# Kernel optimization log

Hardware: AMD Instinct MI355X
Metric: run time of the kernel (lower is better)

## Reference

```python
import jax, jax.numpy as jnp
import numpy as np

BETA = 0.1
TRUNC = 1.0
MIN_VALID_RATIO = 0.3


def _wls_affine(x, y, w):
    # Weighted least squares fit of y ~ s*x + t over the last axis.
    sw = w.sum(-1)
    swx = (w * x).sum(-1)
    swy = (w * y).sum(-1)
    swxx = (w * x * x).sum(-1)
    swxy = (w * x * y).sum(-1)
    det = sw * swxx - swx * swx
    det = jnp.where(jnp.abs(det) < 1e-12, 1e-12, det)
    s = (sw * swxy - swx * swy) / det
    t = (swxx * swy - swx * swxy) / det
    return s, t


def _align_depth_affine(x, y, w, trunc):
    # Truncated robust affine alignment: initial WLS fit, then refit with
    # weights of points whose weighted residual exceeds `trunc` zeroed out
    # (falling back to the original weights if everything is truncated).
    s0, t0 = _wls_affine(x, y, w)
    e = w * jnp.abs(s0[..., None] * x + t0[..., None] - y)
    w2 = w * (e < trunc).astype(w.dtype)
    w2 = jnp.where(w2.sum(-1, keepdims=True) > 1e-8, w2, w)
    return _wls_affine(x, y, w2)


def _smooth(err, beta):
    if beta == 0:
        return err
    return jnp.where(err < beta, 0.5 * err * err / beta, err - 0.5 * beta)


def setup_inputs() -> dict:
    key = jax.random.key(0)
    k1, k2, k3 = jax.random.split(key, 3)
    B = 8
    P = 4096  # num_patches
    K = 256   # patch_pixel_count
    N = P * K
    pred_depth = jax.random.uniform(k1, (B, N), jnp.float32, 0.05, 5.0)
    gt_depth = jax.random.uniform(k2, (B, N), jnp.float32, 0.05, 5.0)
    mask = jax.random.bernoulli(k3, 0.8, (B, N))
    global_scale = jnp.ones((B,), jnp.float32)
    return {
        "pred_depth": pred_depth,
        "gt_depth": gt_depth,
        "mask": mask,
        "global_scale": global_scale,
        "num_patches": P,
        "patch_pixel_count": K,
    }


def reference(pred_depth, gt_depth, mask, global_scale, num_patches, patch_pixel_count):
    B = pred_depth.shape[0]
    P, K = num_patches, patch_pixel_count
    x = pred_depth.reshape(B, P, K)
    y = gt_depth.reshape(B, P, K)
    m = mask.reshape(B, P, K).astype(x.dtype)

    valid_ratio = m.mean(-1)                      # (B, P)
    msum = m.sum(-1)
    mean_depth = jnp.where(msum > 0, (y * m).sum(-1) / jnp.maximum(msum, 1.0), 1.0)

    w = m / jnp.maximum(y, 1e-5)                  # alignment weights (B, P, K)
    s, t = _align_depth_affine(x, y, w, TRUNC)    # (B, P) scale / shift per patch

    ratio = s / jnp.maximum(global_scale[:, None], 1e-12)
    gs_ok = jnp.where(global_scale[:, None] > 0, (ratio >= 0.1) & (ratio <= 10.0), True)
    valid = (valid_ratio >= MIN_VALID_RATIO) & (s > 0) & gs_ok  # (B, P)

    aligned = s[..., None] * x + t[..., None]
    pw = m / jnp.maximum(y, 0.1 * mean_depth[..., None])
    patch_loss = _smooth(jnp.abs(aligned - y) * pw, BETA).mean(-1)  # (B, P)

    vf = valid.astype(x.dtype)
    cnt = vf.sum()
    loss = jnp.where(cnt > 0, (patch_loss * vf).sum() / jnp.maximum(cnt, 1.0), 0.0)
    return loss
```

## Files before the change

### kernel.cpp

```cpp
#include <hip/hip_runtime.h>


#define WPB 4
#define PPW 4
#define MAXBLK 1024

__device__ __forceinline__ float wredu(float v) {
#define DPP_ADD(ctrl)                                                        \
  v += __int_as_float(__builtin_amdgcn_update_dpp(                           \
      0, __float_as_int(v), (ctrl), 0xf, 0xf, true))
  DPP_ADD(0x111);
  DPP_ADD(0x112);
  DPP_ADD(0x114);
  DPP_ADD(0x118);
  DPP_ADD(0x142);
  DPP_ADD(0x143);
#undef DPP_ADD
  return __int_as_float(__builtin_amdgcn_readlane(__float_as_int(v), 63));
}

__device__ __forceinline__ float rowredu(float v) {
#define DPP_ADD(ctrl)                                                        \
  v += __int_as_float(__builtin_amdgcn_update_dpp(                           \
      0, __float_as_int(v), (ctrl), 0xf, 0xf, true))
  DPP_ADD(0x121);
  DPP_ADD(0x122);
  DPP_ADD(0x124);
  DPP_ADD(0x128);
#undef DPP_ADD
  return v;
}

__device__ __forceinline__ float frcp(float x) {
  return __builtin_amdgcn_rcpf(x);
}

__global__ __launch_bounds__(256) void moge_patch_kernel(
    const float* __restrict__ xg,
    const float* __restrict__ yg,
    const int*   __restrict__ mg,
    const float* __restrict__ gsg,
    const int*   __restrict__ pP,
    const int*   __restrict__ pK,
    int B,
    float* __restrict__ ws) {
  const int P = pP[0];
  const int K = pK[0];
  const int lane = threadIdx.x & 63;
  const int wib  = threadIdx.x >> 6;
  const int total_patches = B * P;
  const float invK = 1.0f / (float)K;

  float wloss = 0.f, wcnt = 0.f;

  if (K == 256) {
    const int row = lane >> 4;
    const int col = lane & 15;
    const int poff = col * 16;
    const int wave_stride = gridDim.x * WPB * PPW;

    int pbase = (blockIdx.x * WPB + wib) * PPW;
    if (pbase < total_patches) {
      float4 xa[4], ya[4]; int4 ma[4];
      {
        const int patch0 = pbase + row;
        const long base =
            ((patch0 < total_patches) ? (long)patch0 * 256L : 0L) + poff;
        #pragma unroll
        for (int j = 0; j < 4; ++j) {
          xa[j] = *(const float4*)(xg + base + 4 * j);
          ya[j] = *(const float4*)(yg + base + 4 * j);
          ma[j] = *(const int4*)(mg + base + 4 * j);
        }
      }

      for (;;) {
        const int nbase_p = pbase + wave_stride;
        const bool has_next = nbase_p < total_patches;
        float4 nxa[4], nya[4]; int4 nma[4];
        {
          const int np = nbase_p + row;
          const long nb =
              ((has_next && np < total_patches) ? (long)np * 256L : 0L) + poff;
          #pragma unroll
          for (int j = 0; j < 4; ++j) {
            nxa[j] = *(const float4*)(xg + nb + 4 * j);
            nya[j] = *(const float4*)(yg + nb + 4 * j);
            nma[j] = *(const int4*)(mg + nb + 4 * j);
          }
        }

        const int patch = pbase + row;
        const bool row_ok = patch < total_patches;
        const float* xr = (const float*)xa;
        const float* yr = (const float*)ya;
        const int*   mi = (const int*)ma;
        float wv[16];

        float sw = 0.f, swx = 0.f, swy = 0.f, swxx = 0.f, swxy = 0.f;
        float msum = 0.f, symsum = 0.f;
        #pragma unroll
        for (int i = 0; i < 16; ++i) {
          const float m = mi[i] ? 1.f : 0.f;
          const float xx = xr[i], yy = yr[i];
          const float w = m * frcp(fmaxf(yy, 1e-5f));
          wv[i] = w;
          const float wx = w * xx;
          sw += w; swx += wx; swy = fmaf(w, yy, swy);
          swxx = fmaf(wx, xx, swxx); swxy = fmaf(wx, yy, swxy);
          msum += m; symsum = fmaf(m, yy, symsum);
        }
        sw = rowredu(sw); swx = rowredu(swx); swy = rowredu(swy);
        swxx = rowredu(swxx); swxy = rowredu(swxy);

        float det = sw * swxx - swx * swx;
        if (fabsf(det) < 1e-12f) det = 1e-12f;
        float rdet = frcp(det);
        const float s0 = (sw * swxy - swx * swy) * rdet;
        const float t0 = (swxx * swy - swx * swxy) * rdet;

        float sw2 = 0.f, swx2 = 0.f, swy2 = 0.f, swxx2 = 0.f, swxy2 = 0.f;
        #pragma unroll
        for (int i = 0; i < 16; ++i) {
          const float xx = xr[i], yy = yr[i], w = wv[i];
          const float e = w * fabsf(fmaf(s0, xx, t0) - yy);
          const float w2 = (e < 1.0f) ? w : 0.f;
          const float w2x = w2 * xx;
          sw2 += w2; swx2 += w2x; swy2 = fmaf(w2, yy, swy2);
          swxx2 = fmaf(w2x, xx, swxx2); swxy2 = fmaf(w2x, yy, swxy2);
        }
        sw2 = rowredu(sw2); swx2 = rowredu(swx2); swy2 = rowredu(swy2);
        swxx2 = rowredu(swxx2); swxy2 = rowredu(swxy2);
        msum = rowredu(msum); symsum = rowredu(symsum);

        if (sw2 > 1e-8f) {
          sw = sw2; swx = swx2; swy = swy2; swxx = swxx2; swxy = swxy2;
        }
        det = sw * swxx - swx * swx;
        if (fabsf(det) < 1e-12f) det = 1e-12f;
        rdet = frcp(det);
        const float s = (sw * swxy - swx * swy) * rdet;
        const float t = (swxx * swy - swx * swxy) * rdet;

        const float mean_depth =
            (msum > 0.f) ? (symsum * frcp(fmaxf(msum, 1.f))) : 1.f;
        const float yfloor = 0.1f * mean_depth;

        float lsum = 0.f;
        #pragma unroll
        for (int i = 0; i < 16; ++i) {
          const float m = (wv[i] > 0.f) ? 1.f : 0.f;
          const float pw = m * frcp(fmaxf(yr[i], yfloor));
          const float err = fabsf(fmaf(s, xr[i], t) - yr[i]) * pw;
          lsum += (err < 0.1f) ? (5.0f * err * err) : (err - 0.05f);
        }
        const float patch_loss = rowredu(lsum) * invK;

        const int pidx = row_ok ? patch : (total_patches - 1);
        const float gs = gsg[(unsigned)pidx / (unsigned)P];
        const float ratio = s * frcp(fmaxf(gs, 1e-12f));
        const bool gs_ok = (gs > 0.f) ? (ratio >= 0.1f && ratio <= 10.0f) : true;
        const bool valid = (msum * invK >= 0.3f) && (s > 0.f) && gs_ok;

        if (col == 0 && row_ok && valid) { wloss += patch_loss; wcnt += 1.f; }

        if (!has_next) break;
        pbase = nbase_p;
        #pragma unroll
        for (int j = 0; j < 4; ++j) { xa[j] = nxa[j]; ya[j] = nya[j]; ma[j] = nma[j]; }
      }
    }
  } else {
    const int wave_stride = gridDim.x * WPB;
    for (int patch = blockIdx.x * WPB + wib; patch < total_patches;
         patch += wave_stride) {
      const long base = (long)patch * (long)K;
      const float* xp = xg + base;
      const float* yp = yg + base;
      const int*   mp = mg + base;

      float sw = 0.f, swx = 0.f, swy = 0.f, swxx = 0.f, swxy = 0.f;
      float msum = 0.f, symsum = 0.f;
      for (int j = lane; j < K; j += 64) {
        const float m = mp[j] ? 1.f : 0.f;
        const float xx = xp[j], yy = yp[j];
        const float w = m * frcp(fmaxf(yy, 1e-5f));
        const float wx = w * xx;
        sw += w; swx += wx; swy = fmaf(w, yy, swy);
        swxx = fmaf(wx, xx, swxx); swxy = fmaf(wx, yy, swxy);
        msum += m; symsum = fmaf(m, yy, symsum);
      }
      sw = wredu(sw); swx = wredu(swx); swy = wredu(swy);
      swxx = wredu(swxx); swxy = wredu(swxy);
      msum = wredu(msum); symsum = wredu(symsum);

      float det = sw * swxx - swx * swx;
      if (fabsf(det) < 1e-12f) det = 1e-12f;
      float rdet = frcp(det);
      const float s0 = (sw * swxy - swx * swy) * rdet;
      const float t0 = (swxx * swy - swx * swxy) * rdet;

      float sw2 = 0.f, swx2 = 0.f, swy2 = 0.f, swxx2 = 0.f, swxy2 = 0.f;
      for (int j = lane; j < K; j += 64) {
        const float m = mp[j] ? 1.f : 0.f;
        const float xx = xp[j], yy = yp[j];
        const float w = m * frcp(fmaxf(yy, 1e-5f));
        const float e = w * fabsf(fmaf(s0, xx, t0) - yy);
        const float w2 = (e < 1.0f) ? w : 0.f;
        const float w2x = w2 * xx;
        sw2 += w2; swx2 += w2x; swy2 = fmaf(w2, yy, swy2);
        swxx2 = fmaf(w2x, xx, swxx2); swxy2 = fmaf(w2x, yy, swxy2);
      }
      sw2 = wredu(sw2); swx2 = wredu(swx2); swy2 = wredu(swy2);
      swxx2 = wredu(swxx2); swxy2 = wredu(swxy2);

      if (sw2 > 1e-8f) {
        sw = sw2; swx = swx2; swy = swy2; swxx = swxx2; swxy = swxy2;
      }
      det = sw * swxx - swx * swx;
      if (fabsf(det) < 1e-12f) det = 1e-12f;
      rdet = frcp(det);
      const float s = (sw * swxy - swx * swy) * rdet;
      const float t = (swxx * swy - swx * swxy) * rdet;

      const float mean_depth =
          (msum > 0.f) ? (symsum * frcp(fmaxf(msum, 1.f))) : 1.f;
      const float yfloor = 0.1f * mean_depth;

      float lsum = 0.f;
      for (int j = lane; j < K; j += 64) {
        const float m = mp[j] ? 1.f : 0.f;
        const float xx = xp[j], yy = yp[j];
        const float pw = m * frcp(fmaxf(yy, yfloor));
        const float err = fabsf(fmaf(s, xx, t) - yy) * pw;
        lsum += (err < 0.1f) ? (5.0f * err * err) : (err - 0.05f);
      }
      const float patch_loss = wredu(lsum) * invK;

      const float gs = gsg[(unsigned)patch / (unsigned)P];
      const float ratio = s * frcp(fmaxf(gs, 1e-12f));
      const bool gs_ok = (gs > 0.f) ? (ratio >= 0.1f && ratio <= 10.0f) : true;
      const bool valid = (msum * invK >= 0.3f) && (s > 0.f) && gs_ok;

      if (lane == 0 && valid) { wloss += patch_loss; wcnt += 1.f; }
    }
  }

  wloss = wredu(wloss);
  wcnt  = wredu(wcnt);
  __shared__ float sl[WPB], sc[WPB];
  if (lane == 0) { sl[wib] = wloss; sc[wib] = wcnt; }
  __syncthreads();
  if (threadIdx.x == 0) {
    float bl = 0.f, bc = 0.f;
    #pragma unroll
    for (int i = 0; i < WPB; ++i) { bl += sl[i]; bc += sc[i]; }
    ws[blockIdx.x * 32]     = bl;
    ws[blockIdx.x * 32 + 1] = bc;
  }
}

__global__ __launch_bounds__(256) void finalize_kernel(
    const float* __restrict__ ws, float* __restrict__ out, int nblocks) {
  const int lane = threadIdx.x & 63;
  const int wib  = threadIdx.x >> 6;
  float l = 0.f, c = 0.f;
  for (int i = threadIdx.x; i < nblocks; i += 256) {
    l += ws[i * 32];
    c += ws[i * 32 + 1];
  }
  l = wredu(l); c = wredu(c);
  __shared__ float sl[4], sc[4];
  if (lane == 0) { sl[wib] = l; sc[wib] = c; }
  __syncthreads();
  if (threadIdx.x == 0) {
    const float L = sl[0] + sl[1] + sl[2] + sl[3];
    const float C = sc[0] + sc[1] + sc[2] + sc[3];
    out[0] = (C > 0.f) ? (L / fmaxf(C, 1.f)) : 0.f;
  }
}

extern "C" void kernel_launch(void* const* d_in, const int* in_sizes, int n_in,
                              void* d_out, int out_size, void* d_ws, size_t ws_size,
                              hipStream_t stream) {
  const float* pred = (const float*)d_in[0];
  const float* gt   = (const float*)d_in[1];
  const int*   mask = (const int*)d_in[2];
  const float* gs   = (const float*)d_in[3];
  const int*   pP   = (const int*)d_in[4];
  const int*   pK   = (const int*)d_in[5];
  const int B = in_sizes[3];
  const long total_pixels = (long)in_sizes[0];
  float* ws = (float*)d_ws;

  long est_patches = total_pixels / 256;
  long blocks = (est_patches + WPB * PPW - 1) / (WPB * PPW);
  if (blocks < 1) blocks = 1;
  if (blocks > MAXBLK) blocks = MAXBLK;
  moge_patch_kernel<<<(int)blocks, 256, 0, stream>>>(pred, gt, mask, gs, pP,
                                                     pK, B, ws);
  finalize_kernel<<<1, 256, 0, stream>>>(ws, (float*)d_out, (int)blocks);
}
```

Baseline: 128.5 us.

## Drop register prefetch, pack mask to bits, raise occupancy and grid size

Removes the software double-buffered prefetch of the next patch group, packs the 16 mask ints per lane into a bitmask, and recomputes weights instead of storing a 16-float array. Together with launch_bounds(256,8) and a larger MAXBLK, this cuts register pressure so more waves can be resident and latency is hidden by occupancy rather than explicit prefetch. The cost is extra reciprocal work per element and the loss of explicit load/compute overlap within a wave.

```diff
diff --git a/kernel.cpp b/kernel.cpp
--- a/kernel.cpp
+++ b/kernel.cpp
@@ -3,7 +3,7 @@
 
 #define WPB 4
 #define PPW 4
-#define MAXBLK 1024
+#define MAXBLK 2048
 
 __device__ __forceinline__ float wredu(float v) {
 #define DPP_ADD(ctrl)                                                        \
@@ -35,7 +35,7 @@
   return __builtin_amdgcn_rcpf(x);
 }
 
-__global__ __launch_bounds__(256) void moge_patch_kernel(
+__global__ __launch_bounds__(256, 8) void moge_patch_kernel(
     const float* __restrict__ xg,
     const float* __restrict__ yg,
     const int*   __restrict__ mg,
@@ -57,118 +57,96 @@
     const int row = lane >> 4;
     const int col = lane & 15;
     const int poff = col * 16;
-    const int wave_stride = gridDim.x * WPB * PPW;
-
-    int pbase = (blockIdx.x * WPB + wib) * PPW;
-    if (pbase < total_patches) {
-      float4 xa[4], ya[4]; int4 ma[4];
-      {
-        const int patch0 = pbase + row;
-        const long base =
-            ((patch0 < total_patches) ? (long)patch0 * 256L : 0L) + poff;
-        #pragma unroll
-        for (int j = 0; j < 4; ++j) {
-          xa[j] = *(const float4*)(xg + base + 4 * j);
-          ya[j] = *(const float4*)(yg + base + 4 * j);
-          ma[j] = *(const int4*)(mg + base + 4 * j);
-        }
-      }
-
-      for (;;) {
-        const int nbase_p = pbase + wave_stride;
-        const bool has_next = nbase_p < total_patches;
-        float4 nxa[4], nya[4]; int4 nma[4];
-        {
-          const int np = nbase_p + row;
-          const long nb =
-              ((has_next && np < total_patches) ? (long)np * 256L : 0L) + poff;
-          #pragma unroll
-          for (int j = 0; j < 4; ++j) {
-            nxa[j] = *(const float4*)(xg + nb + 4 * j);
-            nya[j] = *(const float4*)(yg + nb + 4 * j);
-            nma[j] = *(const int4*)(mg + nb + 4 * j);
-          }
-        }
-
-        const int patch = pbase + row;
-        const bool row_ok = patch < total_patches;
-        const float* xr = (const float*)xa;
-        const float* yr = (const float*)ya;
-        const int*   mi = (const int*)ma;
-        float wv[16];
-
-        float sw = 0.f, swx = 0.f, swy = 0.f, swxx = 0.f, swxy = 0.f;
-        float msum = 0.f, symsum = 0.f;
-        #pragma unroll
-        for (int i = 0; i < 16; ++i) {
-          const float m = mi[i] ? 1.f : 0.f;
-          const float xx = xr[i], yy = yr[i];
-          const float w = m * frcp(fmaxf(yy, 1e-5f));
-          wv[i] = w;
-          const float wx = w * xx;
-          sw += w; swx += wx; swy = fmaf(w, yy, swy);
-          swxx = fmaf(wx, xx, swxx); swxy = fmaf(wx, yy, swxy);
-          msum += m; symsum = fmaf(m, yy, symsum);
-        }
-        sw = rowredu(sw); swx = rowredu(swx); swy = rowredu(swy);
-        swxx = rowredu(swxx); swxy = rowredu(swxy);
-
-        float det = sw * swxx - swx * swx;
-        if (fabsf(det) < 1e-12f) det = 1e-12f;
-        float rdet = frcp(det);
-        const float s0 = (sw * swxy - swx * swy) * rdet;
-        const float t0 = (swxx * swy - swx * swxy) * rdet;
-
-        float sw2 = 0.f, swx2 = 0.f, swy2 = 0.f, swxx2 = 0.f, swxy2 = 0.f;
-        #pragma unroll
-        for (int i = 0; i < 16; ++i) {
-          const float xx = xr[i], yy = yr[i], w = wv[i];
-          const float e = w * fabsf(fmaf(s0, xx, t0) - yy);
-          const float w2 = (e < 1.0f) ? w : 0.f;
-          const float w2x = w2 * xx;
-          sw2 += w2; swx2 += w2x; swy2 = fmaf(w2, yy, swy2);
-          swxx2 = fmaf(w2x, xx, swxx2); swxy2 = fmaf(w2x, yy, swxy2);
-        }
-        sw2 = rowredu(sw2); swx2 = rowredu(swx2); swy2 = rowredu(swy2);
-        swxx2 = rowredu(swxx2); swxy2 = rowredu(swxy2);
-        msum = rowredu(msum); symsum = rowredu(symsum);
-
-        if (sw2 > 1e-8f) {
-          sw = sw2; swx = swx2; swy = swy2; swxx = swxx2; swxy = swxy2;
-        }
-        det = sw * swxx - swx * swx;
-        if (fabsf(det) < 1e-12f) det = 1e-12f;
-        rdet = frcp(det);
-        const float s = (sw * swxy - swx * swy) * rdet;
-        const float t = (swxx * swy - swx * swxy) * rdet;
-
-        const float mean_depth =
-            (msum > 0.f) ? (symsum * frcp(fmaxf(msum, 1.f))) : 1.f;
-        const float yfloor = 0.1f * mean_depth;
-
-        float lsum = 0.f;
-        #pragma unroll
-        for (int i = 0; i < 16; ++i) {
-          const float m = (wv[i] > 0.f) ? 1.f : 0.f;
-          const float pw = m * frcp(fmaxf(yr[i], yfloor));
-          const float err = fabsf(fmaf(s, xr[i], t) - yr[i]) * pw;
-          lsum += (err < 0.1f) ? (5.0f * err * err) : (err - 0.05f);
-        }
-        const float patch_loss = rowredu(lsum) * invK;
-
-        const int pidx = row_ok ? patch : (total_patches - 1);
-        const float gs = gsg[(unsigned)pidx / (unsigned)P];
-        const float ratio = s * frcp(fmaxf(gs, 1e-12f));
-        const bool gs_ok = (gs > 0.f) ? (ratio >= 0.1f && ratio <= 10.0f) : true;
-        const bool valid = (msum * invK >= 0.3f) && (s > 0.f) && gs_ok;
-
-        if (col == 0 && row_ok && valid) { wloss += patch_loss; wcnt += 1.f; }
-
-        if (!has_next) break;
-        pbase = nbase_p;
-        #pragma unroll
-        for (int j = 0; j < 4; ++j) { xa[j] = nxa[j]; ya[j] = nya[j]; ma[j] = nma[j]; }
-      }
+    const int group_stride = gridDim.x * WPB * PPW;
+
+    for (int pbase = (blockIdx.x * WPB + wib) * PPW; pbase < total_patches;
+         pbase += group_stride) {
+      const int patch = pbase + row;
+      const bool row_ok = patch < total_patches;
+      const long base = (row_ok ? (long)patch * 256L : 0L) + poff;
+
+      float4 xa[4], ya[4];
+      unsigned mbits = 0;
+      #pragma unroll
+      for (int j = 0; j < 4; ++j) {
+        xa[j] = *(const float4*)(xg + base + 4 * j);
+        ya[j] = *(const float4*)(yg + base + 4 * j);
+        const int4 m4 = *(const int4*)(mg + base + 4 * j);
+        mbits |= (m4.x ? 1u : 0u) << (4 * j);
+        mbits |= (m4.y ? 2u : 0u) << (4 * j);
+        mbits |= (m4.z ? 4u : 0u) << (4 * j);
+        mbits |= (m4.w ? 8u : 0u) << (4 * j);
+      }
+      const float* xr = (const float*)xa;
+      const float* yr = (const float*)ya;
+
+      float sw = 0.f, swx = 0.f, swy = 0.f, swxx = 0.f, swxy = 0.f;
+      float msum = 0.f, symsum = 0.f;
+      #pragma unroll
+      for (int i = 0; i < 16; ++i) {
+        const float m = (mbits >> i) & 1u ? 1.f : 0.f;
+        const float xx = xr[i], yy = yr[i];
+        const float w = m * frcp(fmaxf(yy, 1e-5f));
+        const float wx = w * xx;
+        sw += w; swx += wx; swy = fmaf(w, yy, swy);
+        swxx = fmaf(wx, xx, swxx); swxy = fmaf(wx, yy, swxy);
+        msum += m; symsum = fmaf(m, yy, symsum);
+      }
+      sw = rowredu(sw); swx = rowredu(swx); swy = rowredu(swy);
+      swxx = rowredu(swxx); swxy = rowredu(swxy);
+
+      float det = sw * swxx - swx * swx;
+      if (fabsf(det) < 1e-12f) det = 1e-12f;
+      float rdet = frcp(det);
+      const float s0 = (sw * swxy - swx * swy) * rdet;
+      const float t0 = (swxx * swy - swx * swxy) * rdet;
+
+      float sw2 = 0.f, swx2 = 0.f, swy2 = 0.f, swxx2 = 0.f, swxy2 = 0.f;
+      #pragma unroll
+      for (int i = 0; i < 16; ++i) {
+        const float m = (mbits >> i) & 1u ? 1.f : 0.f;
+        const float xx = xr[i], yy = yr[i];
+        const float w = m * frcp(fmaxf(yy, 1e-5f));
+        const float e = w * fabsf(fmaf(s0, xx, t0) - yy);
+        const float w2 = (e < 1.0f) ? w : 0.f;
+        const float w2x = w2 * xx;
+        sw2 += w2; swx2 += w2x; swy2 = fmaf(w2, yy, swy2);
+        swxx2 = fmaf(w2x, xx, swxx2); swxy2 = fmaf(w2x, yy, swxy2);
+      }
+      sw2 = rowredu(sw2); swx2 = rowredu(swx2); swy2 = rowredu(swy2);
+      swxx2 = rowredu(swxx2); swxy2 = rowredu(swxy2);
+      msum = rowredu(msum); symsum = rowredu(symsum);
+
+      if (sw2 > 1e-8f) {
+        sw = sw2; swx = swx2; swy = swy2; swxx = swxx2; swxy = swxy2;
+      }
+      det = sw * swxx - swx * swx;
+      if (fabsf(det) < 1e-12f) det = 1e-12f;
+      rdet = frcp(det);
+      const float s = (sw * swxy - swx * swy) * rdet;
+      const float t = (swxx * swy - swx * swxy) * rdet;
+
+      const float mean_depth =
+          (msum > 0.f) ? (symsum * frcp(fmaxf(msum, 1.f))) : 1.f;
+      const float yfloor = 0.1f * mean_depth;
+
+      float lsum = 0.f;
+      #pragma unroll
+      for (int i = 0; i < 16; ++i) {
+        const float m = (mbits >> i) & 1u ? 1.f : 0.f;
+        const float pw = m * frcp(fmaxf(yr[i], yfloor));
+        const float err = fabsf(fmaf(s, xr[i], t) - yr[i]) * pw;
+        lsum += (err < 0.1f) ? (5.0f * err * err) : (err - 0.05f);
+      }
+      const float patch_loss = rowredu(lsum) * invK;
+
+      const int pidx = row_ok ? patch : (total_patches - 1);
+      const float gs = gsg[(unsigned)pidx / (unsigned)P];
+      const float ratio = s * frcp(fmaxf(gs, 1e-12f));
+      const bool gs_ok = (gs > 0.f) ? (ratio >= 0.1f && ratio <= 10.0f) : true;
+      const bool valid = (msum * invK >= 0.3f) && (s > 0.f) && gs_ok;
+
+      if (col == 0 && row_ok && valid) { wloss += patch_loss; wcnt += 1.f; }
     }
   } else {
     const int wave_stride = gridDim.x * WPB;
```

Result: slower. 205.9 us (+60.3%).
